# Performance work log

Measured on AMD Instinct MI355X. Metric: run time of the kernel, lower is better.

Reference implementation:

```python
import jax, jax.numpy as jnp
import numpy as np

B, L, D = 2, 2048, 2048
H, HKV, HD = 32, 8, 64
G = H // HKV  # GQA group size


def _rope(t, cos, sin):
    # t: [B, h, L, HD]; cos/sin: [L, HD//2]; pairs are consecutive (view_as_complex)
    tr, ti = t[..., 0::2], t[..., 1::2]
    out_r = tr * cos - ti * sin
    out_i = tr * sin + ti * cos
    return jnp.stack([out_r, out_i], axis=-1).reshape(t.shape)


def setup_inputs() -> dict:
    key = jax.random.key(0)
    ks = jax.random.split(key, 5)
    x = jax.random.normal(ks[0], (B, L, D), dtype=jnp.float32)
    wq = jax.random.normal(ks[1], (D, H * HD), dtype=jnp.float32) * 0.02
    wk = jax.random.normal(ks[2], (D, HKV * HD), dtype=jnp.float32) * 0.02
    wv = jax.random.normal(ks[3], (D, HKV * HD), dtype=jnp.float32) * 0.02
    wo = jax.random.normal(ks[4], (D, D), dtype=jnp.float32) * 0.02
    # RoPE freqs: theta_i = 10000^(-2i/HD), angle[p, i] = p * theta_i
    inv_freq = 1.0 / (10000.0 ** (jnp.arange(0, HD, 2, dtype=jnp.float32) / HD))
    angles = jnp.arange(L, dtype=jnp.float32)[:, None] * inv_freq[None, :]  # [L, HD//2]
    freqs_cos = jnp.cos(angles)
    freqs_sin = jnp.sin(angles)
    # additive causal mask [L, L]
    mask = jnp.where(jnp.tril(jnp.ones((L, L), dtype=bool)), 0.0, -1e9).astype(jnp.float32)
    return {"x": x, "wq": wq, "wk": wk, "wv": wv, "wo": wo,
            "freqs_cos": freqs_cos, "freqs_sin": freqs_sin, "mask": mask}


def reference(x, wq, wk, wv, wo, freqs_cos, freqs_sin, mask):
    b, l, _ = x.shape
    q = (x @ wq).reshape(b, l, H, HD).transpose(0, 2, 1, 3)      # [B, H, L, HD]
    k = (x @ wk).reshape(b, l, HKV, HD).transpose(0, 2, 1, 3)    # [B, HKV, L, HD]
    v = (x @ wv).reshape(b, l, HKV, HD).transpose(0, 2, 1, 3)
    q = _rope(q, freqs_cos, freqs_sin)
    k = _rope(k, freqs_cos, freqs_sin)
    # native GQA broadcast instead of repeat_kv copy (same math)
    qg = q.reshape(b, HKV, G, l, HD)
    scores = jnp.einsum("bhgqd,bhkd->bhgqk", qg, k) / jnp.sqrt(jnp.float32(HD))
    scores = scores + mask  # [B, HKV, G, L, L]
    probs = jax.nn.softmax(scores.astype(jnp.float32), axis=-1).astype(v.dtype)
    out = jnp.einsum("bhgqk,bhkd->bhgqd", probs, v)              # [B, HKV, G, L, HD]
    out = out.reshape(b, H, l, HD).transpose(0, 2, 1, 3).reshape(b, l, H * HD)
    return out @ wo
```

## Files before the change

### kernel.cpp

```cpp
#include <hip/hip_runtime.h>
#include <hip/hip_bf16.h>

#define B_   2
#define L_   2048
#define D_   2048
#define H_   32
#define HKV_ 8
#define HD_  64
#define G_   4
#define M_   4096
#define NF_  3072

typedef __attribute__((ext_vector_type(8))) short bf16x8;
typedef __attribute__((ext_vector_type(4))) float f32x4;

static __device__ __forceinline__ unsigned short f2bf(float f) {
  unsigned int u = __float_as_uint(f);
  unsigned int r = (u + 0x7FFFu + ((u >> 16) & 1u)) >> 16;
  return (unsigned short)r;
}
static __device__ __forceinline__ unsigned short f2bf_hw(float f) {
  __hip_bfloat16 h = __float2bfloat16(f);
  return *(unsigned short*)&h;
}

#define GLD16(g, l) __builtin_amdgcn_global_load_lds(                      \
    (const __attribute__((address_space(1))) void*)(g),                    \
    (__attribute__((address_space(3))) void*)(l), 16, 0, 0)

__global__ void cast_bf16_kernel(const float* __restrict__ in,
                                 unsigned short* __restrict__ out, int n4) {
  int i = blockIdx.x * blockDim.x + threadIdx.x;
  if (i >= n4) return;
  float4 v = ((const float4*)in)[i];
  uint2 r;
  r.x = (unsigned int)f2bf(v.x) | ((unsigned int)f2bf(v.y) << 16);
  r.y = (unsigned int)f2bf(v.z) | ((unsigned int)f2bf(v.w) << 16);
  ((uint2*)out)[i] = r;
}

__global__ void transpose_cast_kernel(const float* __restrict__ src,
                                      unsigned short* __restrict__ dst,
                                      int K, int N) {
  __shared__ float tile[32][33];
  int k0 = blockIdx.y * 32, n0 = blockIdx.x * 32;
  int tx = threadIdx.x, ty = threadIdx.y;
#pragma unroll
  for (int r = 0; r < 4; ++r)
    tile[ty * 4 + r][tx] = src[(size_t)(k0 + ty * 4 + r) * N + n0 + tx];
  __syncthreads();
#pragma unroll
  for (int r = 0; r < 4; ++r)
    dst[(size_t)(n0 + ty * 4 + r) * K + k0 + tx] = f2bf(tile[tx][ty * 4 + r]);
}

__global__ __launch_bounds__(256)
void gemm_bt_kernel(const unsigned short* __restrict__ A,
                    const unsigned short* __restrict__ Bt,
                    float* __restrict__ C, int M, int N, int K) {
  __shared__ unsigned short Al[128 * 32];
  __shared__ unsigned short Bl[128 * 32];
  const int tid = threadIdx.x;
  const int w = tid >> 6;
  const int l = tid & 63;
  const int row0 = blockIdx.y * 128;
  const int col0 = blockIdx.x * 128;
  const int wr = (w >> 1) * 64, wc = (w & 1) * 64;

  f32x4 acc[4][4];
#pragma unroll
  for (int m = 0; m < 4; ++m)
#pragma unroll
    for (int n = 0; n < 4; ++n) acc[m][n] = (f32x4){0.f, 0.f, 0.f, 0.f};

  const int srow = l >> 2;
  const int scol = (l & 3) * 8;
  const int fr = l & 15, fk = (l >> 4) * 8;
  const int nk = K / 32;

  for (int kt = 0; kt < nk; ++kt) {
    const int k0 = kt * 32;
#pragma unroll
    for (int t = 0; t < 2; ++t) {
      const int rr = (w * 2 + t) * 16 + srow;
      GLD16(A + (size_t)(row0 + rr) * K + k0 + scol, &Al[(w * 2 + t) * 512]);
      GLD16(Bt + (size_t)(col0 + rr) * K + k0 + scol, &Bl[(w * 2 + t) * 512]);
    }
    __syncthreads();
    bf16x8 af[4], bfr[4];
#pragma unroll
    for (int m = 0; m < 4; ++m)
      af[m] = *(const bf16x8*)&Al[(wr + m * 16 + fr) * 32 + fk];
#pragma unroll
    for (int n = 0; n < 4; ++n)
      bfr[n] = *(const bf16x8*)&Bl[(wc + n * 16 + fr) * 32 + fk];
#pragma unroll
    for (int m = 0; m < 4; ++m)
#pragma unroll
      for (int n = 0; n < 4; ++n)
        acc[m][n] = __builtin_amdgcn_mfma_f32_16x16x32_bf16(af[m], bfr[n], acc[m][n], 0, 0, 0);
    __syncthreads();
  }

  const int fq = l >> 4;
#pragma unroll
  for (int m = 0; m < 4; ++m)
#pragma unroll
    for (int n = 0; n < 4; ++n)
#pragma unroll
      for (int j = 0; j < 4; ++j) {
        int r = row0 + wr + m * 16 + fq * 4 + j;
        int c = col0 + wc + n * 16 + fr;
        C[(size_t)r * N + c] = acc[m][n][j];
      }
}

__global__ void rope_kernel(const float* __restrict__ src,
                            const float* __restrict__ cosf,
                            const float* __restrict__ sinf,
                            unsigned short* __restrict__ dst, int nh, int col_off,
                            float scale, int total) {
  int idx = blockIdx.x * blockDim.x + threadIdx.x;
  if (idx >= total) return;
  int g = idx & 7;
  int h = (idx >> 3) & (nh - 1);
  int row = idx / (nh << 3);
  int lpos = row & (L_ - 1);
  int b = row >> 11;
  const float* s = src + (size_t)row * NF_ + col_off + h * 64 + g * 8;
  float4 v0 = *(const float4*)s;
  float4 v1 = *(const float4*)(s + 4);
  float4 c4 = *(const float4*)(cosf + lpos * 32 + g * 4);
  float4 s4 = *(const float4*)(sinf + lpos * 32 + g * 4);
  float o0 = (v0.x * c4.x - v0.y * s4.x) * scale;
  float o1 = (v0.x * s4.x + v0.y * c4.x) * scale;
  float o2 = (v0.z * c4.y - v0.w * s4.y) * scale;
  float o3 = (v0.z * s4.y + v0.w * c4.y) * scale;
  float o4 = (v1.x * c4.z - v1.y * s4.z) * scale;
  float o5 = (v1.x * s4.z + v1.y * c4.z) * scale;
  float o6 = (v1.z * c4.w - v1.w * s4.w) * scale;
  float o7 = (v1.z * s4.w + v1.w * c4.w) * scale;
  uint4 r;
  r.x = (unsigned int)f2bf(o0) | ((unsigned int)f2bf(o1) << 16);
  r.y = (unsigned int)f2bf(o2) | ((unsigned int)f2bf(o3) << 16);
  r.z = (unsigned int)f2bf(o4) | ((unsigned int)f2bf(o5) << 16);
  r.w = (unsigned int)f2bf(o6) | ((unsigned int)f2bf(o7) << 16);
  *(uint4*)&dst[(((size_t)(b * nh + h)) * L_ + lpos) * 64 + g * 8] = r;
}

__global__ void cast_vT_kernel(const float* __restrict__ v,
                               unsigned short* __restrict__ vT) {
  __shared__ float tile[32][33];
  int l0 = blockIdx.x * 32, d0 = blockIdx.y * 32;
  int z = blockIdx.z;
  int b = z >> 3, hkv = z & 7;
  int tx = threadIdx.x, ty = threadIdx.y;
  const float* src = v + (size_t)(b * L_) * NF_ + 2560 + hkv * 64;
#pragma unroll
  for (int r = 0; r < 4; ++r)
    tile[ty * 4 + r][tx] = src[(size_t)(l0 + ty * 4 + r) * NF_ + d0 + tx];
  __syncthreads();
  unsigned short* dst = vT + ((size_t)z * 64) * L_;
#pragma unroll
  for (int r = 0; r < 4; ++r)
    dst[(size_t)(d0 + ty * 4 + r) * L_ + l0 + tx] = f2bf(tile[tx][ty * 4 + r]);
}

__global__ __launch_bounds__(256)
void attn_kernel(const unsigned short* __restrict__ Q,
                 const unsigned short* __restrict__ Kt,
                 const unsigned short* __restrict__ Vt,
                 unsigned short* __restrict__ O) {
  __shared__ unsigned short Kl[2][64 * 64];
  __shared__ unsigned short Vl[2][64 * 64];
  __shared__ unsigned short Pl[64 * 64];
  const int tid = threadIdx.x, w = tid >> 6, l = tid & 63;
  const int lin = blockIdx.y * 16 + blockIdx.x;
  const int work = ((lin & 7) << 7) + (lin >> 3);
  const int bh = work >> 4, by = work & 15;
  const int b = bh >> 5, h = bh & 31;
  const int hkv = h >> 2;
  const int q0 = by * 128;
  const int fr = l & 15, hi = l >> 4;
  const int frx = fr & 7;

  const int srow = l >> 3;
  const int scole = ((l & 7) ^ srow) * 8;

  const unsigned short* kbase = Kt + ((size_t)(b * HKV_ + hkv)) * L_ * 64;
  const unsigned short* vbase = Vt + ((size_t)(b * HKV_ + hkv)) * 64 * L_;

  bf16x8 qf[2][2];
#pragma unroll
  for (int s = 0; s < 2; ++s) {
    const unsigned short* qb =
        Q + (((size_t)bh) * L_ + q0 + s * 64 + w * 16 + fr) * 64 + hi * 8;
    qf[s][0] = *(const bf16x8*)(qb);
    qf[s][1] = *(const bf16x8*)(qb + 32);
  }

  float m_i[2][4], l_p[2][4];
  f32x4 oacc[2][4];
#pragma unroll
  for (int s = 0; s < 2; ++s)
#pragma unroll
    for (int j = 0; j < 4; ++j) { m_i[s][j] = -1e30f; l_p[s][j] = 0.f; }
#pragma unroll
  for (int s = 0; s < 2; ++s)
#pragma unroll
    for (int nf = 0; nf < 4; ++nf) oacc[s][nf] = (f32x4){0.f, 0.f, 0.f, 0.f};

  const int nt = 2 * by + 2;

#define ASTAGE(kv0_, buf_) do {                                              \
    _Pragma("unroll")                                                        \
    for (int u_ = 0; u_ < 2; ++u_) {                                         \
      const int c_ = w * 2 + u_;                                             \
      const int rr_ = c_ * 8 + srow;                                         \
      GLD16(kbase + ((size_t)((kv0_) + rr_)) * 64 + scole,                   \
            &Kl[buf_][c_ * 512]);                                            \
      GLD16(vbase + ((size_t)rr_) * L_ + (kv0_) + scole,                     \
            &Vl[buf_][c_ * 512]);                                            \
    }                                                                        \
  } while (0)

  ASTAGE(0, 0);

  for (int t = 0; t < nt; ++t) {
    const int buf = t & 1;
    if (t + 1 < nt) {
      ASTAGE((t + 1) * 64, buf ^ 1);
      asm volatile("s_waitcnt vmcnt(4)" ::: "memory");
    } else {
      asm volatile("s_waitcnt vmcnt(0)" ::: "memory");
    }
    __builtin_amdgcn_s_barrier();

    const int kv0 = t * 64;
#pragma unroll
    for (int s = 0; s < 2; ++s) {
      const int dlim = 2 * by + s;
      if (t > dlim) continue;

      f32x4 sacc[4];
#pragma unroll
      for (int nf = 0; nf < 4; ++nf) sacc[nf] = (f32x4){0.f, 0.f, 0.f, 0.f};
      __builtin_amdgcn_s_setprio(1);
#pragma unroll
      for (int ks = 0; ks < 2; ++ks) {
#pragma unroll
        for (int nf = 0; nf < 4; ++nf) {
          bf16x8 kfrag = *(const bf16x8*)
              &Kl[buf][(nf * 16 + fr) * 64 + (((ks * 4 + hi) ^ frx) * 8)];
          sacc[nf] = __builtin_amdgcn_mfma_f32_16x16x32_bf16(qf[s][ks], kfrag, sacc[nf], 0, 0, 0);
        }
      }
      __builtin_amdgcn_s_setprio(0);

      if (t == dlim) {
        const int rbase = q0 + s * 64 + w * 16 + hi * 4;
#pragma unroll
        for (int nf = 0; nf < 4; ++nf)
#pragma unroll
          for (int j = 0; j < 4; ++j)
            if (kv0 + nf * 16 + fr > rbase + j) sacc[nf][j] = -1e30f;
      }

      float rowmax[4];
#pragma unroll
      for (int j = 0; j < 4; ++j) {
        float mx = fmaxf(fmaxf(sacc[0][j], sacc[1][j]),
                         fmaxf(sacc[2][j], sacc[3][j]));
        mx = fmaxf(mx, __shfl_xor(mx, 1));
        mx = fmaxf(mx, __shfl_xor(mx, 2));
        mx = fmaxf(mx, __shfl_xor(mx, 4));
        mx = fmaxf(mx, __shfl_xor(mx, 8));
        rowmax[j] = mx;
      }

      float g = rowmax[0] - m_i[s][0];
      g = fmaxf(g, rowmax[1] - m_i[s][1]);
      g = fmaxf(g, rowmax[2] - m_i[s][2]);
      g = fmaxf(g, rowmax[3] - m_i[s][3]);
      if (!__all(g <= 8.f)) {
#pragma unroll
        for (int j = 0; j < 4; ++j) {
          float mnew = fmaxf(m_i[s][j], rowmax[j]);
          float cr = exp2f(m_i[s][j] - mnew);
          m_i[s][j] = mnew;
          l_p[s][j] *= cr;
#pragma unroll
          for (int nf = 0; nf < 4; ++nf) oacc[s][nf][j] *= cr;
        }
      }

#pragma unroll
      for (int j = 0; j < 4; ++j) {
        const int prow = w * 16 + hi * 4 + j;
#pragma unroll
        for (int nf = 0; nf < 4; ++nf) {
          float p = exp2f(sacc[nf][j] - m_i[s][j]);
          l_p[s][j] += p;
          Pl[prow * 64 + (((nf * 2 + (fr >> 3)) ^ (prow & 7)) * 8) + frx] =
              f2bf_hw(p);
        }
      }

      __builtin_amdgcn_s_setprio(1);
#pragma unroll
      for (int ks = 0; ks < 2; ++ks) {
        bf16x8 pa = *(const bf16x8*)
            &Pl[(w * 16 + fr) * 64 + (((ks * 4 + hi) ^ frx) * 8)];
#pragma unroll
        for (int nf = 0; nf < 4; ++nf) {
          bf16x8 vfrag = *(const bf16x8*)
              &Vl[buf][(nf * 16 + fr) * 64 + (((ks * 4 + hi) ^ frx) * 8)];
          oacc[s][nf] = __builtin_amdgcn_mfma_f32_16x16x32_bf16(pa, vfrag, oacc[s][nf], 0, 0, 0);
        }
      }
      __builtin_amdgcn_s_setprio(0);
    }
    __builtin_amdgcn_s_barrier();
  }
#undef ASTAGE

#pragma unroll
  for (int s = 0; s < 2; ++s)
#pragma unroll
    for (int j = 0; j < 4; ++j) {
      float lsum = l_p[s][j];
      lsum += __shfl_xor(lsum, 1);
      lsum += __shfl_xor(lsum, 2);
      lsum += __shfl_xor(lsum, 4);
      lsum += __shfl_xor(lsum, 8);
      float inv = 1.0f / lsum;
#pragma unroll
      for (int nf = 0; nf < 4; ++nf) {
        int qrow = q0 + s * 64 + w * 16 + hi * 4 + j;
        int d = nf * 16 + fr;
        O[((size_t)(b * L_ + qrow)) * 2048 + h * 64 + d] =
            f2bf_hw(oacc[s][nf][j] * inv);
      }
    }
}

extern "C" void kernel_launch(void* const* d_in, const int* in_sizes, int n_in,
                              void* d_out, int out_size, void* d_ws, size_t ws_size,
                              hipStream_t stream) {
  (void)in_sizes; (void)n_in; (void)out_size; (void)ws_size;
  const float* x  = (const float*)d_in[0];
  const float* wq = (const float*)d_in[1];
  const float* wk = (const float*)d_in[2];
  const float* wv = (const float*)d_in[3];
  const float* wo = (const float*)d_in[4];
  const float* fc = (const float*)d_in[5];
  const float* fs = (const float*)d_in[6];
  float* out = (float*)d_out;

  char* ws = (char*)d_ws;
  unsigned short* x_b  = (unsigned short*)(ws + 0);
  unsigned short* wT   = (unsigned short*)(ws + 16777216);
  unsigned short* woT  = (unsigned short*)(ws + 29360128);
  float* qkv_f         = (float*)(ws + 37748736);
  unsigned short* at_b = (unsigned short*)(ws + 37748736);
  unsigned short* q_b  = (unsigned short*)(ws + 88080384);
  unsigned short* k_b  = (unsigned short*)(ws + 104857600);
  unsigned short* vT_b = (unsigned short*)(ws + 109051904);

  const float qscale = 0.125f * 1.4426950408889634f;

  dim3 tb(32, 8);
  cast_bf16_kernel<<<8192, 256, 0, stream>>>(x, x_b, M_ * D_ / 4);
  transpose_cast_kernel<<<dim3(64, 64), tb, 0, stream>>>(wq, wT, 2048, 2048);
  transpose_cast_kernel<<<dim3(16, 64), tb, 0, stream>>>(wk, wT + (size_t)2048 * 2048, 2048, 512);
  transpose_cast_kernel<<<dim3(16, 64), tb, 0, stream>>>(wv, wT + (size_t)2560 * 2048, 2048, 512);
  transpose_cast_kernel<<<dim3(64, 64), tb, 0, stream>>>(wo, woT, 2048, 2048);

  gemm_bt_kernel<<<dim3(24, 32), 256, 0, stream>>>(x_b, wT, qkv_f, M_, NF_, 2048);

  rope_kernel<<<4096, 256, 0, stream>>>(qkv_f, fc, fs, q_b, 32, 0, qscale, M_ * 32 * 8);
  rope_kernel<<<1024, 256, 0, stream>>>(qkv_f, fc, fs, k_b, 8, 2048, 1.0f, M_ * 8 * 8);
  cast_vT_kernel<<<dim3(64, 2, 16), tb, 0, stream>>>(qkv_f, vT_b);

  attn_kernel<<<dim3(16, 64), 256, 0, stream>>>(q_b, k_b, vT_b, at_b);

  gemm_bt_kernel<<<dim3(16, 32), 256, 0, stream>>>(at_b, woT, out, M_, 2048, 2048);
}
```

Before: 449.4 us.

## Double-buffer 256x128 GEMM, pair causal attention tiles, fuse QKV weight transposes

Replaces the 128x128 GEMM with a 512-thread 256x128-tile kernel that double-buffers LDS, prefetching the next K slice while MFMAs run, with raised wave priority around the MFMA block. Attention blocks now each process two causal query tiles (pr and 15-pr), which balances work per block and halves the grid. The three QKV weight transpose launches become one kernel. These aim to overlap loads with compute and even out causal imbalance, at the cost of a doubled LDS footprint in the GEMM and fewer, longer attention blocks.

```diff
diff --git a/kernel.cpp b/kernel.cpp
--- a/kernel.cpp
+++ b/kernel.cpp
@@ -54,18 +54,40 @@
     dst[(size_t)(n0 + ty * 4 + r) * K + k0 + tx] = f2bf(tile[tx][ty * 4 + r]);
 }
 
-__global__ __launch_bounds__(256)
-void gemm_bt_kernel(const unsigned short* __restrict__ A,
-                    const unsigned short* __restrict__ Bt,
-                    float* __restrict__ C, int M, int N, int K) {
-  __shared__ unsigned short Al[128 * 32];
-  __shared__ unsigned short Bl[128 * 32];
+__global__ void transpose_cast_qkv_kernel(const float* __restrict__ wq,
+                                          const float* __restrict__ wk,
+                                          const float* __restrict__ wv,
+                                          unsigned short* __restrict__ dst) {
+  __shared__ float tile[32][33];
+  int n0 = blockIdx.x * 32, k0 = blockIdx.y * 32;
+  const float* src;
+  int ns, N;
+  if (n0 < 2048)      { src = wq; ns = n0;        N = 2048; }
+  else if (n0 < 2560) { src = wk; ns = n0 - 2048; N = 512; }
+  else                { src = wv; ns = n0 - 2560; N = 512; }
+  int tx = threadIdx.x, ty = threadIdx.y;
+#pragma unroll
+  for (int r = 0; r < 4; ++r)
+    tile[ty * 4 + r][tx] = src[(size_t)(k0 + ty * 4 + r) * N + ns + tx];
+  __syncthreads();
+#pragma unroll
+  for (int r = 0; r < 4; ++r)
+    dst[(size_t)(n0 + ty * 4 + r) * 2048 + k0 + tx] = f2bf(tile[tx][ty * 4 + r]);
+}
+
+__global__ __launch_bounds__(512)
+void gemm256x128_kernel(const unsigned short* __restrict__ A,
+                        const unsigned short* __restrict__ Bt,
+                        float* __restrict__ C, int M, int N, int K) {
+  __shared__ unsigned short Al[2][256 * 32];
+  __shared__ unsigned short Bl[2][128 * 32];
   const int tid = threadIdx.x;
-  const int w = tid >> 6;
-  const int l = tid & 63;
-  const int row0 = blockIdx.y * 128;
-  const int col0 = blockIdx.x * 128;
-  const int wr = (w >> 1) * 64, wc = (w & 1) * 64;
+  const int w = tid >> 6, l = tid & 63;
+  const int wave_m = w >> 1, wave_n = w & 1;
+  const int row0 = blockIdx.y * 256, col0 = blockIdx.x * 128;
+  const int fr = l & 15, fk = (l >> 4) * 8;
+  const int srow = l >> 2, scol = (l & 3) * 8;
+  const int nk = K >> 5;
 
   f32x4 acc[4][4];
 #pragma unroll
@@ -73,34 +95,44 @@
 #pragma unroll
     for (int n = 0; n < 4; ++n) acc[m][n] = (f32x4){0.f, 0.f, 0.f, 0.f};
 
-  const int srow = l >> 2;
-  const int scol = (l & 3) * 8;
-  const int fr = l & 15, fk = (l >> 4) * 8;
-  const int nk = K / 32;
+#define GSTAGE(buf_, kt_) do {                                               \
+    GLD16(A + (size_t)(row0 + w * 16 + srow) * K + (kt_) * 32 + scol,        \
+          &Al[buf_][w * 512]);                                               \
+    GLD16(A + (size_t)(row0 + 128 + w * 16 + srow) * K + (kt_) * 32 + scol,  \
+          &Al[buf_][(8 + w) * 512]);                                         \
+    GLD16(Bt + (size_t)(col0 + w * 16 + srow) * K + (kt_) * 32 + scol,       \
+          &Bl[buf_][w * 512]);                                               \
+  } while (0)
+
+  GSTAGE(0, 0);
 
   for (int kt = 0; kt < nk; ++kt) {
-    const int k0 = kt * 32;
-#pragma unroll
-    for (int t = 0; t < 2; ++t) {
-      const int rr = (w * 2 + t) * 16 + srow;
-      GLD16(A + (size_t)(row0 + rr) * K + k0 + scol, &Al[(w * 2 + t) * 512]);
-      GLD16(Bt + (size_t)(col0 + rr) * K + k0 + scol, &Bl[(w * 2 + t) * 512]);
+    const int buf = kt & 1;
+    if (kt + 1 < nk) {
+      GSTAGE(buf ^ 1, kt + 1);
+      asm volatile("s_waitcnt vmcnt(3)" ::: "memory");
+    } else {
+      asm volatile("s_waitcnt vmcnt(0)" ::: "memory");
     }
-    __syncthreads();
+    __builtin_amdgcn_s_barrier();
+
     bf16x8 af[4], bfr[4];
 #pragma unroll
     for (int m = 0; m < 4; ++m)
-      af[m] = *(const bf16x8*)&Al[(wr + m * 16 + fr) * 32 + fk];
+      af[m] = *(const bf16x8*)&Al[buf][(wave_m * 64 + m * 16 + fr) * 32 + fk];
 #pragma unroll
     for (int n = 0; n < 4; ++n)
-      bfr[n] = *(const bf16x8*)&Bl[(wc + n * 16 + fr) * 32 + fk];
+      bfr[n] = *(const bf16x8*)&Bl[buf][(wave_n * 64 + n * 16 + fr) * 32 + fk];
+    __builtin_amdgcn_s_setprio(1);
 #pragma unroll
     for (int m = 0; m < 4; ++m)
 #pragma unroll
       for (int n = 0; n < 4; ++n)
         acc[m][n] = __builtin_amdgcn_mfma_f32_16x16x32_bf16(af[m], bfr[n], acc[m][n], 0, 0, 0);
-    __syncthreads();
+    __builtin_amdgcn_s_setprio(0);
+    __builtin_amdgcn_s_barrier();
   }
+#undef GSTAGE
 
   const int fq = l >> 4;
 #pragma unroll
@@ -109,8 +141,8 @@
     for (int n = 0; n < 4; ++n)
 #pragma unroll
       for (int j = 0; j < 4; ++j) {
-        int r = row0 + wr + m * 16 + fq * 4 + j;
-        int c = col0 + wc + n * 16 + fr;
+        int r = row0 + wave_m * 64 + m * 16 + fq * 4 + j;
+        int c = col0 + wave_n * 64 + n * 16 + fr;
         C[(size_t)r * N + c] = acc[m][n][j];
       }
 }
@@ -175,12 +207,11 @@
   __shared__ unsigned short Vl[2][64 * 64];
   __shared__ unsigned short Pl[64 * 64];
   const int tid = threadIdx.x, w = tid >> 6, l = tid & 63;
-  const int lin = blockIdx.y * 16 + blockIdx.x;
-  const int work = ((lin & 7) << 7) + (lin >> 3);
-  const int bh = work >> 4, by = work & 15;
+  const int lin = blockIdx.y * 8 + blockIdx.x;
+  const int work = ((lin & 7) << 6) + (lin >> 3);
+  const int bh = work >> 3, pr = work & 7;
   const int b = bh >> 5, h = bh & 31;
   const int hkv = h >> 2;
-  const int q0 = by * 128;
   const int fr = l & 15, hi = l >> 4;
   const int frx = fr & 7;
 
@@ -189,28 +220,6 @@
 
   const unsigned short* kbase = Kt + ((size_t)(b * HKV_ + hkv)) * L_ * 64;
   const unsigned short* vbase = Vt + ((size_t)(b * HKV_ + hkv)) * 64 * L_;
-
-  bf16x8 qf[2][2];
-#pragma unroll
-  for (int s = 0; s < 2; ++s) {
-    const unsigned short* qb =
-        Q + (((size_t)bh) * L_ + q0 + s * 64 + w * 16 + fr) * 64 + hi * 8;
-    qf[s][0] = *(const bf16x8*)(qb);
-    qf[s][1] = *(const bf16x8*)(qb + 32);
-  }
-
-  float m_i[2][4], l_p[2][4];
-  f32x4 oacc[2][4];
-#pragma unroll
-  for (int s = 0; s < 2; ++s)
-#pragma unroll
-    for (int j = 0; j < 4; ++j) { m_i[s][j] = -1e30f; l_p[s][j] = 0.f; }
-#pragma unroll
-  for (int s = 0; s < 2; ++s)
-#pragma unroll
-    for (int nf = 0; nf < 4; ++nf) oacc[s][nf] = (f32x4){0.f, 0.f, 0.f, 0.f};
-
-  const int nt = 2 * by + 2;
 
 #define ASTAGE(kv0_, buf_) do {                                              \
     _Pragma("unroll")                                                        \
@@ -224,124 +233,151 @@
     }                                                                        \
   } while (0)
 
-  ASTAGE(0, 0);
-
-  for (int t = 0; t < nt; ++t) {
-    const int buf = t & 1;
-    if (t + 1 < nt) {
-      ASTAGE((t + 1) * 64, buf ^ 1);
-      asm volatile("s_waitcnt vmcnt(4)" ::: "memory");
-    } else {
-      asm volatile("s_waitcnt vmcnt(0)" ::: "memory");
+  for (int half = 0; half < 2; ++half) {
+    const int by = half ? (15 - pr) : pr;
+    const int q0 = by * 128;
+
+    bf16x8 qf[2][2];
+#pragma unroll
+    for (int s = 0; s < 2; ++s) {
+      const unsigned short* qb =
+          Q + (((size_t)bh) * L_ + q0 + s * 64 + w * 16 + fr) * 64 + hi * 8;
+      qf[s][0] = *(const bf16x8*)(qb);
+      qf[s][1] = *(const bf16x8*)(qb + 32);
     }
-    __builtin_amdgcn_s_barrier();
-
-    const int kv0 = t * 64;
-#pragma unroll
-    for (int s = 0; s < 2; ++s) {
-      const int dlim = 2 * by + s;
-      if (t > dlim) continue;
-
-      f32x4 sacc[4];
-#pragma unroll
-      for (int nf = 0; nf < 4; ++nf) sacc[nf] = (f32x4){0.f, 0.f, 0.f, 0.f};
-      __builtin_amdgcn_s_setprio(1);
-#pragma unroll
-      for (int ks = 0; ks < 2; ++ks) {
+
+    float m_i[2][4], l_p[2][4];
+    f32x4 oacc[2][4];
+#pragma unroll
+    for (int s = 0; s < 2; ++s)
+#pragma unroll
+      for (int j = 0; j < 4; ++j) { m_i[s][j] = -1e30f; l_p[s][j] = 0.f; }
+#pragma unroll
+    for (int s = 0; s < 2; ++s)
+#pragma unroll
+      for (int nf = 0; nf < 4; ++nf) oacc[s][nf] = (f32x4){0.f, 0.f, 0.f, 0.f};
+
+    const int nt = 2 * by + 2;
+
+    ASTAGE(0, 0);
+
+    for (int t = 0; t < nt; ++t) {
+      const int buf = t & 1;
+      if (t + 1 < nt) {
+        ASTAGE((t + 1) * 64, buf ^ 1);
+        asm volatile("s_waitcnt vmcnt(4)" ::: "memory");
+      } else {
+        asm volatile("s_waitcnt vmcnt(0)" ::: "memory");
+      }
+      __builtin_amdgcn_s_barrier();
+
+      const int kv0 = t * 64;
+#pragma unroll
+      for (int s = 0; s < 2; ++s) {
+        const int dlim = 2 * by + s;
+        if (t > dlim) continue;
+
+        f32x4 sacc[4];
+#pragma unroll
+        for (int nf = 0; nf < 4; ++nf) sacc[nf] = (f32x4){0.f, 0.f, 0.f, 0.f};
+        __builtin_amdgcn_s_setprio(1);
+#pragma unroll
+        for (int ks = 0; ks < 2; ++ks) {
+#pragma unroll
+          for (int nf = 0; nf < 4; ++nf) {
+            bf16x8 kfrag = *(const bf16x8*)
+                &Kl[buf][(nf * 16 + fr) * 64 + (((ks * 4 + hi) ^ frx) * 8)];
+            sacc[nf] = __builtin_amdgcn_mfma_f32_16x16x32_bf16(qf[s][ks], kfrag, sacc[nf], 0, 0, 0);
+          }
+        }
+        __builtin_amdgcn_s_setprio(0);
+
+        if (t == dlim) {
+          const int rbase = q0 + s * 64 + w * 16 + hi * 4;
+#pragma unroll
+          for (int nf = 0; nf < 4; ++nf)
+#pragma unroll
+            for (int j = 0; j < 4; ++j)
+              if (kv0 + nf * 16 + fr > rbase + j) sacc[nf][j] = -1e30f;
+        }
+
+        float rowmax[4];
+#pragma unroll
+        for (int j = 0; j < 4; ++j) {
+          float mx = fmaxf(fmaxf(sacc[0][j], sacc[1][j]),
+                           fmaxf(sacc[2][j], sacc[3][j]));
+          mx = fmaxf(mx, __shfl_xor(mx, 1));
+          mx = fmaxf(mx, __shfl_xor(mx, 2));
+          mx = fmaxf(mx, __shfl_xor(mx, 4));
+          mx = fmaxf(mx, __shfl_xor(mx, 8));
+          rowmax[j] = mx;
+        }
+
+        float g = rowmax[0] - m_i[s][0];
+        g = fmaxf(g, rowmax[1] - m_i[s][1]);
+        g = fmaxf(g, rowmax[2] - m_i[s][2]);
+        g = fmaxf(g, rowmax[3] - m_i[s][3]);
+        if (!__all(g <= 8.f)) {
+#pragma unroll
+          for (int j = 0; j < 4; ++j) {
+            float mnew = fmaxf(m_i[s][j], rowmax[j]);
+            float cr = exp2f(m_i[s][j] - mnew);
+            m_i[s][j] = mnew;
+            l_p[s][j] *= cr;
+#pragma unroll
+            for (int nf = 0; nf < 4; ++nf) oacc[s][nf][j] *= cr;
+          }
+        }
+
+#pragma unroll
+        for (int j = 0; j < 4; ++j) {
+          const int prow = w * 16 + hi * 4 + j;
+#pragma unroll
+          for (int nf = 0; nf < 4; ++nf) {
+            float pv = exp2f(sacc[nf][j] - m_i[s][j]);
+            l_p[s][j] += pv;
+            Pl[prow * 64 + (((nf * 2 + (fr >> 3)) ^ (prow & 7)) * 8) + frx] =
+                f2bf_hw(pv);
+          }
+        }
+
+        __builtin_amdgcn_s_setprio(1);
+#pragma unroll
+        for (int ks = 0; ks < 2; ++ks) {
+          bf16x8 pa = *(const bf16x8*)
+              &Pl[(w * 16 + fr) * 64 + (((ks * 4 + hi) ^ frx) * 8)];
+#pragma unroll
+          for (int nf = 0; nf < 4; ++nf) {
+            bf16x8 vfrag = *(const bf16x8*)
+                &Vl[buf][(nf * 16 + fr) * 64 + (((ks * 4 + hi) ^ frx) * 8)];
+            oacc[s][nf] = __builtin_amdgcn_mfma_f32_16x16x32_bf16(pa, vfrag, oacc[s][nf], 0, 0, 0);
+          }
+        }
+        __builtin_amdgcn_s_setprio(0);
+      }
+      __builtin_amdgcn_s_barrier();
+    }
+
+#pragma unroll
+    for (int s = 0; s < 2; ++s)
+#pragma unroll
+      for (int j = 0; j < 4; ++j) {
+        float lsum = l_p[s][j];
+        lsum += __shfl_xor(lsum, 1);
+        lsum += __shfl_xor(lsum, 2);
+        lsum += __shfl_xor(lsum, 4);
+        lsum += __shfl_xor(lsum, 8);
+        float inv = 1.0f / lsum;
 #pragma unroll
         for (int nf = 0; nf < 4; ++nf) {
-          bf16x8 kfrag = *(const bf16x8*)
-              &Kl[buf][(nf * 16 + fr) * 64 + (((ks * 4 + hi) ^ frx) * 8)];
-          sacc[nf] = __builtin_amdgcn_mfma_f32_16x16x32_bf16(qf[s][ks], kfrag, sacc[nf], 0, 0, 0);
+          int qrow = q0 + s * 64 + w * 16 + hi * 4 + j;
+          int d = nf * 16 + fr;
+          O[((size_t)(b * L_ + qrow)) * 2048 + h * 64 + d] =
+              f2bf_hw(oacc[s][nf][j] * inv);
         }
       }
-      __builtin_amdgcn_s_setprio(0);
-
-      if (t == dlim) {
-        const int rbase = q0 + s * 64 + w * 16 + hi * 4;
-#pragma unroll
-        for (int nf = 0; nf < 4; ++nf)
-#pragma unroll
-          for (int j = 0; j < 4; ++j)
-            if (kv0 + nf * 16 + fr > rbase + j) sacc[nf][j] = -1e30f;
-      }
-
-      float rowmax[4];
-#pragma unroll
-      for (int j = 0; j < 4; ++j) {
-        float mx = fmaxf(fmaxf(sacc[0][j], sacc[1][j]),
-                         fmaxf(sacc[2][j], sacc[3][j]));
-        mx = fmaxf(mx, __shfl_xor(mx, 1));
-        mx = fmaxf(mx, __shfl_xor(mx, 2));
-        mx = fmaxf(mx, __shfl_xor(mx, 4));
-        mx = fmaxf(mx, __shfl_xor(mx, 8));
-        rowmax[j] = mx;
-      }
-
-      float g = rowmax[0] - m_i[s][0];
-      g = fmaxf(g, rowmax[1] - m_i[s][1]);
-      g = fmaxf(g, rowmax[2] - m_i[s][2]);
-      g = fmaxf(g, rowmax[3] - m_i[s][3]);
-      if (!__all(g <= 8.f)) {
-#pragma unroll
-        for (int j = 0; j < 4; ++j) {
-          float mnew = fmaxf(m_i[s][j], rowmax[j]);
-          float cr = exp2f(m_i[s][j] - mnew);
-          m_i[s][j] = mnew;
-          l_p[s][j] *= cr;
-#pragma unroll
-          for (int nf = 0; nf < 4; ++nf) oacc[s][nf][j] *= cr;
-        }
-      }
-
-#pragma unroll
-      for (int j = 0; j < 4; ++j) {
-        const int prow = w * 16 + hi * 4 + j;
-#pragma unroll
-        for (int nf = 0; nf < 4; ++nf) {
-          float p = exp2f(sacc[nf][j] - m_i[s][j]);
-          l_p[s][j] += p;
-          Pl[prow * 64 + (((nf * 2 + (fr >> 3)) ^ (prow & 7)) * 8) + frx] =
-              f2bf_hw(p);
-        }
-      }
-
-      __builtin_amdgcn_s_setprio(1);
-#pragma unroll
-      for (int ks = 0; ks < 2; ++ks) {
-        bf16x8 pa = *(const bf16x8*)
-            &Pl[(w * 16 + fr) * 64 + (((ks * 4 + hi) ^ frx) * 8)];
-#pragma unroll
-        for (int nf = 0; nf < 4; ++nf) {
-          bf16x8 vfrag = *(const bf16x8*)
-              &Vl[buf][(nf * 16 + fr) * 64 + (((ks * 4 + hi) ^ frx) * 8)];
-          oacc[s][nf] = __builtin_amdgcn_mfma_f32_16x16x32_bf16(pa, vfrag, oacc[s][nf], 0, 0, 0);
-        }
-      }
-      __builtin_amdgcn_s_setprio(0);
-    }
-    __builtin_amdgcn_s_barrier();
   }
 #undef ASTAGE
-
-#pragma unroll
-  for (int s = 0; s < 2; ++s)
-#pragma unroll
-    for (int j = 0; j < 4; ++j) {
-      float lsum = l_p[s][j];
-      lsum += __shfl_xor(lsum, 1);
-      lsum += __shfl_xor(lsum, 2);
-      lsum += __shfl_xor(lsum, 4);
-      lsum += __shfl_xor(lsum, 8);
-      float inv = 1.0f / lsum;
-#pragma unroll
-      for (int nf = 0; nf < 4; ++nf) {
-        int qrow = q0 + s * 64 + w * 16 + hi * 4 + j;
-        int d = nf * 16 + fr;
-        O[((size_t)(b * L_ + qrow)) * 2048 + h * 64 + d] =
-            f2bf_hw(oacc[s][nf][j] * inv);
-      }
-    }
 }
 
 extern "C" void kernel_launch(void* const* d_in, const int* in_sizes, int n_in,
@@ -371,18 +407,18 @@
 
   dim3 tb(32, 8);
   cast_bf16_kernel<<<8192, 256, 0, stream>>>(x, x_b, M_ * D_ / 4);
-  transpose_cast_kernel<<<dim3(64, 64), tb, 0, stream>>>(wq, wT, 2048, 2048);
-  transpose_cast_kernel<<<dim3(16, 64), tb, 0, stream>>>(wk, wT + (size_t)2048 * 2048, 2048, 512);
-  transpose_cast_kernel<<<dim3(16, 64), tb, 0, stream>>>(wv, wT + (size_t)2560 * 2048, 2048, 512);
+  transpose_cast_qkv_kernel<<<dim3(96, 64), tb, 0, stream>>>(wq, wk, wv, wT);
   transpose_cast_kernel<<<dim3(64, 64), tb, 0, stream>>>(wo, woT, 2048, 2048);
 
-  gemm_bt_kernel<<<dim3(24, 32), 256, 0, stream>>>(x_b, wT, qkv_f, M_, NF_, 2048);
+  gemm256x128_kernel<<<dim3(NF_ / 128, M_ / 256), 512, 0, stream>>>(
+      x_b, wT, qkv_f, M_, NF_, 2048);
 
   rope_kernel<<<4096, 256, 0, stream>>>(qkv_f, fc, fs, q_b, 32, 0, qscale, M_ * 32 * 8);
   rope_kernel<<<1024, 256, 0, stream>>>(qkv_f, fc, fs, k_b, 8, 2048, 1.0f, M_ * 8 * 8);
   cast_vT_kernel<<<dim3(64, 2, 16), tb, 0, stream>>>(qkv_f, vT_b);
 
-  attn_kernel<<<dim3(16, 64), 256, 0, stream>>>(q_b, k_b, vT_b, at_b);
-
-  gemm_bt_kernel<<<dim3(16, 32), 256, 0, stream>>>(at_b, woT, out, M_, 2048, 2048);
-}
+  attn_kernel<<<dim3(8, 64), 256, 0, stream>>>(q_b, k_b, vT_b, at_b);
+
+  gemm256x128_kernel<<<dim3(2048 / 128, M_ / 256), 512, 0, stream>>>(
+      at_b, woT, out, M_, 2048, 2048);
+}
```

After: 387.4 us. -13.8%, faster.
